# Optimization experiments

Measured on AMD Instinct MI355X. Metric: run time of the kernel, lower is better.

## Reference

```python
import jax, jax.numpy as jnp
import numpy as np

MODEL_DIM = 1024
BATCH, SEQ = 4, 2048


def setup_inputs() -> dict:
    key = jax.random.key(0)
    kx, kq, kk, kv = jax.random.split(key, 4)
    s = 1.0 / np.sqrt(MODEL_DIM)
    return {
        "x": jax.random.normal(kx, (BATCH, SEQ, MODEL_DIM), dtype=jnp.float32),
        "Wq": jax.random.normal(kq, (MODEL_DIM, MODEL_DIM), dtype=jnp.float32) * s,
        "Wk": jax.random.normal(kk, (MODEL_DIM, MODEL_DIM), dtype=jnp.float32) * s,
        "Wv": jax.random.normal(kv, (MODEL_DIM, MODEL_DIM), dtype=jnp.float32) * s,
    }


def reference(x, Wq, Wk, Wv):
    # nn.Linear(d, d, bias=False): y = x @ W.T ; W stored [out, in]
    q = jnp.einsum("bsd,ed->bse", x, Wq)
    k = jnp.einsum("bsd,ed->bse", x, Wk)
    v = jnp.einsum("bsd,ed->bse", x, Wv)
    scores = jnp.einsum("bqd,bkd->bqk", q, k) / jnp.sqrt(jnp.float32(MODEL_DIM))
    attn = jax.nn.softmax(scores, axis=-1)
    return jnp.einsum("bqk,bkd->bqd", attn, v)
```

## Files before the change

kernel.cpp:

```cpp
#include <hip/hip_runtime.h>
#include <hip/hip_bf16.h>


typedef short bf16x8_t __attribute__((ext_vector_type(8)));
typedef float f32x4_t __attribute__((ext_vector_type(4)));
typedef unsigned short u16x8_t __attribute__((ext_vector_type(8)));

static __device__ __forceinline__ unsigned short f2bf(float f) {
  __hip_bfloat16 h = __float2bfloat16(f);
  return *reinterpret_cast<unsigned short*>(&h);
}

#define GLOAD_LDS16(gp, lp)                                            \
  __builtin_amdgcn_global_load_lds(                                    \
      (const __attribute__((address_space(1))) void*)(gp),             \
      (__attribute__((address_space(3))) void*)(lp), 16, 0, 0)

__global__ __launch_bounds__(256) void cast_f32_bf16(
    const float* __restrict__ in, unsigned short* __restrict__ out, int n8) {
  int i = blockIdx.x * 256 + threadIdx.x;
  if (i >= n8) return;
  float4 a = ((const float4*)in)[i * 2];
  float4 b = ((const float4*)in)[i * 2 + 1];
  u16x8_t o;
  o[0] = f2bf(a.x); o[1] = f2bf(a.y); o[2] = f2bf(a.z); o[3] = f2bf(a.w);
  o[4] = f2bf(b.x); o[5] = f2bf(b.y); o[6] = f2bf(b.z); o[7] = f2bf(b.w);
  ((u16x8_t*)out)[i] = o;
}

__global__ __launch_bounds__(256) void cast_w3(
    const float* __restrict__ Wq, const float* __restrict__ Wk,
    const float* __restrict__ Wv, unsigned short* __restrict__ Wqk,
    unsigned short* __restrict__ Wvb) {
  int i = blockIdx.x * 256 + threadIdx.x;
  int seg = i >> 17;
  int local = i & 131071;
  const float* src = (seg == 0) ? Wq : ((seg == 1) ? Wk : Wv);
  unsigned short* dst =
      (seg == 0) ? Wqk : ((seg == 1) ? (Wqk + 1048576) : Wvb);
  float4 a = ((const float4*)src)[local * 2];
  float4 b = ((const float4*)src)[local * 2 + 1];
  u16x8_t o;
  o[0] = f2bf(a.x); o[1] = f2bf(a.y); o[2] = f2bf(a.z); o[3] = f2bf(a.w);
  o[4] = f2bf(b.x); o[5] = f2bf(b.y); o[6] = f2bf(b.z); o[7] = f2bf(b.w);
  ((u16x8_t*)dst)[local] = o;
}

__global__ __launch_bounds__(256) void zero_f32(float* __restrict__ p, int n) {
  int i = blockIdx.x * 256 + threadIdx.x;
  if (i < n) p[i] = 0.0f;
}

template <int EPI, int BN>
__global__ __launch_bounds__(512, 2) void gemm256p(
    const unsigned short* __restrict__ A, const unsigned short* __restrict__ B,
    void* __restrict__ Cv, float* __restrict__ rowsum, int K, int lda,
    int ldb, int ldc, long long sA, long long sB, long long sC, float alpha,
    int rsz) {
  constexpr int NBG = BN / 64;
  constexpr int NH = NBG / 2;
  constexpr int BL = BN / 128;
  constexpr int BNW = BN / 4;
  constexpr int ASZ = 256 * 64;
  constexpr int BSZ = BN * 64;

  __shared__ unsigned short lds[2][ASZ + BSZ];

  const int gx = gridDim.x, gy = gridDim.y;
  const int nwg = gx * gy * gridDim.z;
  const int orig = (blockIdx.z * gy + blockIdx.y) * gx + blockIdx.x;
  const int swz = (orig & 7) * (nwg >> 3) + (orig >> 3);
  const int bx = swz % gx;
  const int tmp = swz / gx;
  const int by = tmp % gy;
  const int z = tmp / gy;

  const int tid = threadIdx.x;
  const int lane = tid & 63;
  const int w = tid >> 6;
  const int wm = w >> 2, wn = w & 3;
  const int m0 = by * 256, n0 = bx * BN;

  A += (long long)z * sA;
  B += (long long)z * sB;

  int sta_row[2][2], sta_col[2][2], sta_lds[2][2];
#pragma unroll
  for (int mh = 0; mh < 2; ++mh)
#pragma unroll
    for (int i = 0; i < 2; ++i) {
      int j = w * 2 + i;
      int l0 = (j >> 3) * 1024 + mh * 512 + (j & 7) * 64;
      int lf = l0 + lane;
      int R = lf >> 3;
      sta_row[mh][i] = R;
      sta_col[mh][i] = ((lf & 7) ^ (R & 7)) * 8;
      sta_lds[mh][i] = l0 * 8;
    }
  int stb_row[2][BL], stb_col[2][BL], stb_lds[2][BL];
#pragma unroll
  for (int nh = 0; nh < 2; ++nh)
#pragma unroll
    for (int i = 0; i < BL; ++i) {
      int l0;
      if (BL == 2) {
        int j = w * 2 + i;
        l0 = (j >> 2) * 512 + nh * 256 + (j & 3) * 64;
      } else {
        int j = w;
        l0 = (j >> 1) * 256 + nh * 128 + (j & 1) * 64;
      }
      int lf = l0 + lane;
      int R = lf >> 3;
      stb_row[nh][i] = R;
      stb_col[nh][i] = ((lf & 7) ^ (R & 7)) * 8;
      stb_lds[nh][i] = ASZ + l0 * 8;
    }

  const int q = lane >> 4, rl = lane & 15;
  int aoff[8][2], boff[NBG][2];
#pragma unroll
  for (int tt = 0; tt < 8; ++tt)
#pragma unroll
    for (int ks = 0; ks < 2; ++ks) {
      int ra = wm * 128 + tt * 16 + rl;
      aoff[tt][ks] = ra * 64 + (((ks * 4 + q) ^ (ra & 7)) * 8);
    }
#pragma unroll
  for (int u = 0; u < NBG; ++u)
#pragma unroll
    for (int ks = 0; ks < 2; ++ks) {
      int rb = wn * BNW + u * 16 + rl;
      boff[u][ks] = ASZ + rb * 64 + (((ks * 4 + q) ^ (rb & 7)) * 8);
    }

  f32x4_t acc[8][NBG];
#pragma unroll
  for (int i = 0; i < 8; ++i)
#pragma unroll
    for (int j = 0; j < NBG; ++j) acc[i][j] = (f32x4_t){0.f, 0.f, 0.f, 0.f};

#define SA(BUFI, MH, K0)                                                    \
  {                                                                         \
    _Pragma("unroll") for (int i_ = 0; i_ < 2; ++i_)                        \
        GLOAD_LDS16(&A[(long long)(m0 + sta_row[MH][i_]) * lda + (K0) +     \
                       sta_col[MH][i_]],                                    \
                    &lds[BUFI][sta_lds[MH][i_]]);                           \
  }
#define SB(BUFI, NH_, K0)                                                   \
  {                                                                         \
    _Pragma("unroll") for (int i_ = 0; i_ < BL; ++i_)                       \
        GLOAD_LDS16(&B[(long long)(n0 + stb_row[NH_][i_]) * ldb + (K0) +    \
                       stb_col[NH_][i_]],                                   \
                    &lds[BUFI][stb_lds[NH_][i_]]);                          \
  }
#define LDAF(MH)                                                            \
  _Pragma("unroll") for (int i_ = 0; i_ < 4; ++i_)                          \
  _Pragma("unroll") for (int ks_ = 0; ks_ < 2; ++ks_)                       \
      af[i_][ks_] = *(const bf16x8_t*)&L[aoff[(MH)*4 + i_][ks_]];
#define LDBG(NH_)                                                           \
  _Pragma("unroll") for (int j_ = 0; j_ < NH; ++j_)                         \
  _Pragma("unroll") for (int ks_ = 0; ks_ < 2; ++ks_)                       \
      bg[j_][ks_] = *(const bf16x8_t*)&L[boff[(NH_)*NH + j_][ks_]];
#define PH_MFMA(MH, NH_)                                                    \
  __builtin_amdgcn_s_barrier();                                             \
  asm volatile("s_waitcnt lgkmcnt(0)" ::: "memory");                        \
  __builtin_amdgcn_sched_barrier(0);                                        \
  __builtin_amdgcn_s_setprio(1);                                            \
  _Pragma("unroll") for (int ks_ = 0; ks_ < 2; ++ks_)                       \
  _Pragma("unroll") for (int i_ = 0; i_ < 4; ++i_)                          \
  _Pragma("unroll") for (int j_ = 0; j_ < NH; ++j_)                         \
      acc[(MH)*4 + i_][(NH_)*NH + j_] =                                     \
          __builtin_amdgcn_mfma_f32_16x16x32_bf16(                          \
              af[i_][ks_], bg[j_][ks_], acc[(MH)*4 + i_][(NH_)*NH + j_],    \
              0, 0, 0);                                                     \
  __builtin_amdgcn_s_setprio(0);                                            \
  __builtin_amdgcn_sched_barrier(0);                                        \
  __builtin_amdgcn_s_barrier();                                             \
  __builtin_amdgcn_sched_barrier(0);

  const int NT = K >> 6;

  SA(0, 0, 0); SA(0, 1, 0); SB(0, 0, 0); SB(0, 1, 0);
  SA(1, 0, 64); SB(1, 1, 64);
  if (BL == 2)
    asm volatile("s_waitcnt vmcnt(4)" ::: "memory");
  else
    asm volatile("s_waitcnt vmcnt(3)" ::: "memory");
  __builtin_amdgcn_s_barrier();
  __builtin_amdgcn_sched_barrier(0);

  bf16x8_t af[4][2], bg[NH][2];

  for (int t = 0; t < NT; ++t) {
    const int bu = t & 1, nx = bu ^ 1;
    const unsigned short* L = lds[bu];
    const bool p1 = (t + 1 < NT), p2 = (t + 2 < NT);
    LDAF(0);
    LDBG(0);
    if (p1) SA(nx, 1, (t + 1) * 64);
    PH_MFMA(0, 0);
    LDBG(1);
    if (p1) SB(nx, 0, (t + 1) * 64);
    PH_MFMA(0, 1);
    LDAF(1);
    if (p2) SA(bu, 0, (t + 2) * 64);
    PH_MFMA(1, 1);
    LDBG(0);
    if (p2) {
      SB(bu, 1, (t + 2) * 64);
      if (BL == 2)
        asm volatile("s_waitcnt vmcnt(4)" ::: "memory");
      else
        asm volatile("s_waitcnt vmcnt(3)" ::: "memory");
    } else {
      asm volatile("s_waitcnt vmcnt(0)" ::: "memory");
    }
    PH_MFMA(1, 0);
  }

  if (EPI == 0) {
    unsigned short* C = (unsigned short*)Cv + (long long)z * sC;
#pragma unroll
    for (int tt = 0; tt < 8; ++tt)
#pragma unroll
      for (int u = 0; u < NBG; ++u)
#pragma unroll
        for (int j = 0; j < 4; ++j) {
          int row = m0 + wm * 128 + tt * 16 + q * 4 + j;
          int col = n0 + wn * BNW + u * 16 + rl;
          C[(long long)row * ldc + col] = f2bf(acc[tt][u][j] * alpha);
        }
  } else if (EPI == 1) {
    unsigned short* C = (unsigned short*)Cv + (long long)z * sC;
#pragma unroll
    for (int tt = 0; tt < 8; ++tt)
#pragma unroll
      for (int j = 0; j < 4; ++j) {
        int row = m0 + wm * 128 + tt * 16 + q * 4 + j;
        float sum = 0.f;
#pragma unroll
        for (int u = 0; u < NBG; ++u) {
          float e = __expf(acc[tt][u][j] * alpha);
          int col = n0 + wn * BNW + u * 16 + rl;
          C[(long long)row * ldc + col] = f2bf(e);
          sum += e;
        }
#pragma unroll
        for (int mk = 1; mk <= 8; mk <<= 1) sum += __shfl_xor(sum, mk);
        if (rl == 0) atomicAdd(&rowsum[z * rsz + row], sum);
      }
  } else {
    float* C = (float*)Cv + (long long)z * sC;
#pragma unroll
    for (int tt = 0; tt < 8; ++tt)
#pragma unroll
      for (int j = 0; j < 4; ++j) {
        int row = m0 + wm * 128 + tt * 16 + q * 4 + j;
        float inv = 1.0f / rowsum[z * rsz + row];
#pragma unroll
        for (int u = 0; u < NBG; ++u) {
          int col = n0 + wn * BNW + u * 16 + rl;
          C[(long long)row * ldc + col] = acc[tt][u][j] * inv;
        }
      }
  }
#undef SA
#undef SB
#undef LDAF
#undef LDBG
#undef PH_MFMA
}

__global__ __launch_bounds__(256) void gemm_nt128(
    const unsigned short* __restrict__ A, const unsigned short* __restrict__ B,
    unsigned short* __restrict__ C, int K, int lda, int ldb, int ldc) {
  __shared__ unsigned short As[128 * 64];
  __shared__ unsigned short Bs[128 * 64];

  const int gx = gridDim.x, gy = gridDim.y;
  const int nwg = gx * gy;
  const int orig = blockIdx.y * gx + blockIdx.x;
  const int swz = (orig & 7) * (nwg >> 3) + (orig >> 3);
  const int bx = swz % gx;
  const int by = swz / gx;

  const int tid = threadIdx.x;
  const int lane = tid & 63;
  const int w = tid >> 6;
  const int wm = w >> 1, wn = w & 1;
  const int m0 = by * 128;
  const int n0 = bx * 128;

  int srow[4], scol[4];
#pragma unroll
  for (int i = 0; i < 4; ++i) {
    int p = w * 256 + i * 64 + lane;
    int r = p >> 3;
    srow[i] = r;
    scol[i] = ((p & 7) ^ (r & 7)) * 8;
  }

  const int q = lane >> 4, rl = lane & 15;
  int aoff[4][2], boff[4][2];
#pragma unroll
  for (int t = 0; t < 4; ++t)
#pragma unroll
    for (int ks = 0; ks < 2; ++ks) {
      int ra = wm * 64 + t * 16 + rl;
      int ca = ks * 4 + q;
      aoff[t][ks] = ra * 64 + ((ca ^ (ra & 7)) * 8);
      int rb = wn * 64 + t * 16 + rl;
      boff[t][ks] = rb * 64 + ((ca ^ (rb & 7)) * 8);
    }

  f32x4_t acc[4][4];
#pragma unroll
  for (int i = 0; i < 4; ++i)
#pragma unroll
    for (int j = 0; j < 4; ++j) acc[i][j] = (f32x4_t){0.f, 0.f, 0.f, 0.f};

  for (int k0 = 0; k0 < K; k0 += 64) {
    __syncthreads();
#pragma unroll
    for (int i = 0; i < 4; ++i) {
      GLOAD_LDS16(&A[(long long)(m0 + srow[i]) * lda + k0 + scol[i]],
                  &As[(w * 4 + i) * 512]);
      GLOAD_LDS16(&B[(long long)(n0 + srow[i]) * ldb + k0 + scol[i]],
                  &Bs[(w * 4 + i) * 512]);
    }
    __syncthreads();

#pragma unroll
    for (int ks = 0; ks < 2; ++ks) {
      bf16x8_t af[4], bgv[4];
#pragma unroll
      for (int t = 0; t < 4; ++t) af[t] = *(const bf16x8_t*)&As[aoff[t][ks]];
#pragma unroll
      for (int u = 0; u < 4; ++u) bgv[u] = *(const bf16x8_t*)&Bs[boff[u][ks]];
#pragma unroll
      for (int i = 0; i < 4; ++i)
#pragma unroll
        for (int j = 0; j < 4; ++j)
          acc[i][j] = __builtin_amdgcn_mfma_f32_16x16x32_bf16(
              af[i], bgv[j], acc[i][j], 0, 0, 0);
    }
  }

#pragma unroll
  for (int t = 0; t < 4; ++t)
#pragma unroll
    for (int u = 0; u < 4; ++u)
#pragma unroll
      for (int j = 0; j < 4; ++j) {
        int row = m0 + wm * 64 + t * 16 + q * 4 + j;
        int col = n0 + wn * 64 + u * 16 + rl;
        C[(long long)row * ldc + col] = f2bf(acc[t][u][j]);
      }
}

extern "C" void kernel_launch(void* const* d_in, const int* in_sizes, int n_in,
                              void* d_out, int out_size, void* d_ws,
                              size_t ws_size, hipStream_t stream) {
  const float* x = (const float*)d_in[0];
  const float* Wq = (const float*)d_in[1];
  const float* Wk = (const float*)d_in[2];
  const float* Wv = (const float*)d_in[3];
  float* out = (float*)d_out;

  unsigned short* xb = (unsigned short*)d_ws;
  unsigned short* Wqk = xb + 8388608;
  unsigned short* Wvb = Wqk + 2097152;
  unsigned short* Cqk = Wvb + 1048576;
  unsigned short* VTb = Cqk + 16777216;
  unsigned short* Scb = VTb + 8388608;
  float* rowsumf = (float*)(Scb + 16777216);

  const dim3 blk(256);
  const dim3 blk512(512);

  cast_f32_bf16<<<4096, blk, 0, stream>>>(x, xb, 1048576);
  cast_w3<<<1536, blk, 0, stream>>>(Wq, Wk, Wv, Wqk, Wvb);
  zero_f32<<<32, blk, 0, stream>>>(rowsumf, 8192);

  gemm256p<0, 256><<<dim3(8, 32, 1), blk512, 0, stream>>>(
      xb, Wqk, Cqk, nullptr, 1024, 1024, 1024, 2048, 0, 0, 0, 1.0f, 0);

  gemm_nt128<<<dim3(64, 8), blk, 0, stream>>>(Wvb, xb, VTb, 1024, 1024, 1024,
                                              8192);

  gemm256p<1, 256><<<dim3(8, 8, 4), blk512, 0, stream>>>(
      Cqk, Cqk + 1024, Scb, rowsumf, 1024, 2048, 2048, 2048,
      (long long)2048 * 2048, (long long)2048 * 2048, (long long)2048 * 2048,
      0.03125f, 2048);

  gemm256p<2, 128><<<dim3(8, 8, 4), blk512, 0, stream>>>(
      Scb, VTb, out, rowsumf, 2048, 2048, 8192, 1024,
      (long long)2048 * 2048, 2048, (long long)2048 * 1024, 1.0f, 2048);
}
```

Measured before the change: 164.0 us.

## Software-pipeline LDS fragment reads across phases and fold rowsum zeroing into weight cast

The GEMM main loop is restructured so LDS fragment reads for the next phase, and for the next K-tile, are issued before the current phase's MFMAs. It uses extra register buffers (afA/afB, bgX0/bgX1/bgY), a loop unrolled by two, and one barrier per phase instead of two. The aim is to hide LDS read latency behind MFMA work and cut barrier overhead. Prefetch addresses wrap modulo NT, so the last tiles issue redundant loads, and the loop assumes NT is even. The separate zero_f32 launch is also removed by zeroing rowsum in extra blocks of cast_w3, saving one kernel launch. The extra register buffers raise register pressure.

```diff
diff --git a/kernel.cpp b/kernel.cpp
--- a/kernel.cpp
+++ b/kernel.cpp
@@ -31,9 +31,18 @@
 __global__ __launch_bounds__(256) void cast_w3(
     const float* __restrict__ Wq, const float* __restrict__ Wk,
     const float* __restrict__ Wv, unsigned short* __restrict__ Wqk,
-    unsigned short* __restrict__ Wvb) {
+    unsigned short* __restrict__ Wvb, float* __restrict__ rowsum) {
   int i = blockIdx.x * 256 + threadIdx.x;
   int seg = i >> 17;
+  if (seg >= 3) {
+    int l = i - 393216;
+    if (l < 1024) {
+      float4 z = {0.f, 0.f, 0.f, 0.f};
+      ((float4*)rowsum)[l * 2] = z;
+      ((float4*)rowsum)[l * 2 + 1] = z;
+    }
+    return;
+  }
   int local = i & 131071;
   const float* src = (seg == 0) ? Wq : ((seg == 1) ? Wk : Wv);
   unsigned short* dst =
@@ -44,11 +53,6 @@
   o[0] = f2bf(a.x); o[1] = f2bf(a.y); o[2] = f2bf(a.z); o[3] = f2bf(a.w);
   o[4] = f2bf(b.x); o[5] = f2bf(b.y); o[6] = f2bf(b.z); o[7] = f2bf(b.w);
   ((u16x8_t*)dst)[local] = o;
-}
-
-__global__ __launch_bounds__(256) void zero_f32(float* __restrict__ p, int n) {
-  int i = blockIdx.x * 256 + threadIdx.x;
-  if (i < n) p[i] = 0.0f;
 }
 
 template <int EPI, int BN>
@@ -140,6 +144,8 @@
 #pragma unroll
     for (int j = 0; j < NBG; ++j) acc[i][j] = (f32x4_t){0.f, 0.f, 0.f, 0.f};
 
+  bf16x8_t afA[4][2], afB[4][2], bgY[NH][2], bgX0[NH][2], bgX1[NH][2];
+
 #define SA(BUFI, MH, K0)                                                    \
   {                                                                         \
     _Pragma("unroll") for (int i_ = 0; i_ < 2; ++i_)                        \
@@ -154,17 +160,15 @@
                        stb_col[NH_][i_]],                                   \
                     &lds[BUFI][stb_lds[NH_][i_]]);                          \
   }
-#define LDAF(MH)                                                            \
+#define RD_AF(DST, L, MH)                                                   \
   _Pragma("unroll") for (int i_ = 0; i_ < 4; ++i_)                          \
   _Pragma("unroll") for (int ks_ = 0; ks_ < 2; ++ks_)                       \
-      af[i_][ks_] = *(const bf16x8_t*)&L[aoff[(MH)*4 + i_][ks_]];
-#define LDBG(NH_)                                                           \
+      DST[i_][ks_] = *(const bf16x8_t*)&(L)[aoff[(MH)*4 + i_][ks_]];
+#define RD_BG(DST, L, NH_)                                                  \
   _Pragma("unroll") for (int j_ = 0; j_ < NH; ++j_)                         \
   _Pragma("unroll") for (int ks_ = 0; ks_ < 2; ++ks_)                       \
-      bg[j_][ks_] = *(const bf16x8_t*)&L[boff[(NH_)*NH + j_][ks_]];
-#define PH_MFMA(MH, NH_)                                                    \
-  __builtin_amdgcn_s_barrier();                                             \
-  asm volatile("s_waitcnt lgkmcnt(0)" ::: "memory");                        \
+      DST[j_][ks_] = *(const bf16x8_t*)&(L)[boff[(NH_)*NH + j_][ks_]];
+#define MM(MH, NH_, AF, BG)                                                 \
   __builtin_amdgcn_sched_barrier(0);                                        \
   __builtin_amdgcn_s_setprio(1);                                            \
   _Pragma("unroll") for (int ks_ = 0; ks_ < 2; ++ks_)                       \
@@ -172,52 +176,65 @@
   _Pragma("unroll") for (int j_ = 0; j_ < NH; ++j_)                         \
       acc[(MH)*4 + i_][(NH_)*NH + j_] =                                     \
           __builtin_amdgcn_mfma_f32_16x16x32_bf16(                          \
-              af[i_][ks_], bg[j_][ks_], acc[(MH)*4 + i_][(NH_)*NH + j_],    \
+              AF[i_][ks_], BG[j_][ks_], acc[(MH)*4 + i_][(NH_)*NH + j_],    \
               0, 0, 0);                                                     \
-  __builtin_amdgcn_s_setprio(0);                                            \
-  __builtin_amdgcn_sched_barrier(0);                                        \
-  __builtin_amdgcn_s_barrier();                                             \
+  __builtin_amdgcn_s_setprio(0);
+
+#define VMC_PH1()                                                           \
+  if constexpr (BL == 2) {                                                  \
+    asm volatile("s_waitcnt vmcnt(4)" ::: "memory");                        \
+  } else {                                                                  \
+    asm volatile("s_waitcnt vmcnt(3)" ::: "memory");                        \
+  }                                                                         \
   __builtin_amdgcn_sched_barrier(0);
+#define VMC_PH2()                                                           \
+  asm volatile("s_waitcnt vmcnt(2)" ::: "memory");                          \
+  __builtin_amdgcn_sched_barrier(0);
+
+#define TILE(T, BU, NX, BGXc, BGXn)                                         \
+  {                                                                         \
+    const unsigned short* Lb = lds[BU];                                     \
+    const unsigned short* Ln = lds[NX];                                     \
+    const int k1 = (((T) + 1 < NT) ? ((T) + 1) : ((T) + 1 - NT)) * 64;      \
+    const int k2 = (((T) + 2 < NT) ? ((T) + 2) : ((T) + 2 - NT)) * 64;      \
+                                                                   \
+    __builtin_amdgcn_s_barrier();                                           \
+    RD_BG(bgY, Lb, 1);                                                      \
+    SA(NX, 1, k1);                                                          \
+    MM(0, 0, afA, BGXc);                                                    \
+                                                                   \
+    __builtin_amdgcn_s_barrier();                                           \
+    RD_AF(afB, Lb, 1);                                                      \
+    SB(NX, 0, k1);                                                          \
+    MM(0, 1, afA, bgY);                                                     \
+    VMC_PH1();                                                              \
+                                                                   \
+    __builtin_amdgcn_s_barrier();                                           \
+    RD_AF(afA, Ln, 0);                                                      \
+    SA(BU, 0, k2);                                                          \
+    MM(1, 1, afB, bgY);                                                     \
+    VMC_PH2();                                                              \
+                                                                   \
+    __builtin_amdgcn_s_barrier();                                           \
+    RD_BG(BGXn, Ln, 0);                                                     \
+    SB(BU, 1, k2);                                                          \
+    MM(1, 0, afB, BGXc);                                                    \
+  }
 
   const int NT = K >> 6;
 
   SA(0, 0, 0); SA(0, 1, 0); SB(0, 0, 0); SB(0, 1, 0);
   SA(1, 0, 64); SB(1, 1, 64);
-  if (BL == 2)
-    asm volatile("s_waitcnt vmcnt(4)" ::: "memory");
-  else
-    asm volatile("s_waitcnt vmcnt(3)" ::: "memory");
+  VMC_PH1();
   __builtin_amdgcn_s_barrier();
-  __builtin_amdgcn_sched_barrier(0);
-
-  bf16x8_t af[4][2], bg[NH][2];
-
-  for (int t = 0; t < NT; ++t) {
-    const int bu = t & 1, nx = bu ^ 1;
-    const unsigned short* L = lds[bu];
-    const bool p1 = (t + 1 < NT), p2 = (t + 2 < NT);
-    LDAF(0);
-    LDBG(0);
-    if (p1) SA(nx, 1, (t + 1) * 64);
-    PH_MFMA(0, 0);
-    LDBG(1);
-    if (p1) SB(nx, 0, (t + 1) * 64);
-    PH_MFMA(0, 1);
-    LDAF(1);
-    if (p2) SA(bu, 0, (t + 2) * 64);
-    PH_MFMA(1, 1);
-    LDBG(0);
-    if (p2) {
-      SB(bu, 1, (t + 2) * 64);
-      if (BL == 2)
-        asm volatile("s_waitcnt vmcnt(4)" ::: "memory");
-      else
-        asm volatile("s_waitcnt vmcnt(3)" ::: "memory");
-    } else {
-      asm volatile("s_waitcnt vmcnt(0)" ::: "memory");
-    }
-    PH_MFMA(1, 0);
-  }
+  RD_AF(afA, lds[0], 0);
+  RD_BG(bgX0, lds[0], 0);
+
+  for (int t = 0; t < NT; t += 2) {
+    TILE(t, 0, 1, bgX0, bgX1);
+    TILE(t + 1, 1, 0, bgX1, bgX0);
+  }
+  asm volatile("s_waitcnt vmcnt(0)" ::: "memory");
 
   if (EPI == 0) {
     unsigned short* C = (unsigned short*)Cv + (long long)z * sC;
@@ -267,9 +284,12 @@
   }
 #undef SA
 #undef SB
-#undef LDAF
-#undef LDBG
-#undef PH_MFMA
+#undef RD_AF
+#undef RD_BG
+#undef MM
+#undef VMC_PH1
+#undef VMC_PH2
+#undef TILE
 }
 
 __global__ __launch_bounds__(256) void gemm_nt128(
@@ -380,8 +400,7 @@
   const dim3 blk512(512);
 
   cast_f32_bf16<<<4096, blk, 0, stream>>>(x, xb, 1048576);
-  cast_w3<<<1536, blk, 0, stream>>>(Wq, Wk, Wv, Wqk, Wvb);
-  zero_f32<<<32, blk, 0, stream>>>(rowsumf, 8192);
+  cast_w3<<<1540, blk, 0, stream>>>(Wq, Wk, Wv, Wqk, Wvb, rowsumf);
 
   gemm256p<0, 256><<<dim3(8, 32, 1), blk512, 0, stream>>>(
       xb, Wqk, Cqk, nullptr, 1024, 1024, 1024, 2048, 0, 0, 0, 1.0f, 0);
```

After: 308.2 us. 87.9% more time.

## Fuse cast/zero kernels and restructure GEMM prefetch with deeper vmcnt waits

Applied to the files above, without the earlier changes.

Merges the x cast, weight cast and rowsum zeroing into one launch to cut launch overhead. In the main GEMM the K loop is unrolled by two with a TILE macro, the order of A/B half-tile prefetches is changed, and the global-load waits move to a looser vmcnt placed mid-tile, so more loads stay in flight across MFMA phases. The risk is that a wrong vmcnt count lets the kernel read LDS data that has not arrived yet. The unrolled loop also assumes the tile count NT is even.

```diff
diff --git a/kernel.cpp b/kernel.cpp
--- a/kernel.cpp
+++ b/kernel.cpp
@@ -16,39 +16,39 @@
       (const __attribute__((address_space(1))) void*)(gp),             \
       (__attribute__((address_space(3))) void*)(lp), 16, 0, 0)
 
-__global__ __launch_bounds__(256) void cast_f32_bf16(
-    const float* __restrict__ in, unsigned short* __restrict__ out, int n8) {
+__global__ __launch_bounds__(256) void cast_all(
+    const float* __restrict__ x, const float* __restrict__ Wq,
+    const float* __restrict__ Wk, const float* __restrict__ Wv,
+    unsigned short* __restrict__ xb, unsigned short* __restrict__ Wqk,
+    unsigned short* __restrict__ Wvb, float* __restrict__ rowsum) {
   int i = blockIdx.x * 256 + threadIdx.x;
-  if (i >= n8) return;
-  float4 a = ((const float4*)in)[i * 2];
-  float4 b = ((const float4*)in)[i * 2 + 1];
-  u16x8_t o;
-  o[0] = f2bf(a.x); o[1] = f2bf(a.y); o[2] = f2bf(a.z); o[3] = f2bf(a.w);
-  o[4] = f2bf(b.x); o[5] = f2bf(b.y); o[6] = f2bf(b.z); o[7] = f2bf(b.w);
-  ((u16x8_t*)out)[i] = o;
-}
-
-__global__ __launch_bounds__(256) void cast_w3(
-    const float* __restrict__ Wq, const float* __restrict__ Wk,
-    const float* __restrict__ Wv, unsigned short* __restrict__ Wqk,
-    unsigned short* __restrict__ Wvb) {
-  int i = blockIdx.x * 256 + threadIdx.x;
-  int seg = i >> 17;
-  int local = i & 131071;
-  const float* src = (seg == 0) ? Wq : ((seg == 1) ? Wk : Wv);
-  unsigned short* dst =
-      (seg == 0) ? Wqk : ((seg == 1) ? (Wqk + 1048576) : Wvb);
+  const float* src;
+  unsigned short* dst;
+  int local;
+  if (i < 1048576) {
+    src = x; dst = xb; local = i;
+  } else {
+    int j = i - 1048576;
+    int seg = j >> 17;
+    if (seg >= 3) {
+      int l = j - 393216;
+      if (l < 1024) {
+        float4 zz = {0.f, 0.f, 0.f, 0.f};
+        ((float4*)rowsum)[l * 2] = zz;
+        ((float4*)rowsum)[l * 2 + 1] = zz;
+      }
+      return;
+    }
+    local = j & 131071;
+    src = (seg == 0) ? Wq : ((seg == 1) ? Wk : Wv);
+    dst = (seg == 0) ? Wqk : ((seg == 1) ? (Wqk + 1048576) : Wvb);
+  }
   float4 a = ((const float4*)src)[local * 2];
   float4 b = ((const float4*)src)[local * 2 + 1];
   u16x8_t o;
   o[0] = f2bf(a.x); o[1] = f2bf(a.y); o[2] = f2bf(a.z); o[3] = f2bf(a.w);
   o[4] = f2bf(b.x); o[5] = f2bf(b.y); o[6] = f2bf(b.z); o[7] = f2bf(b.w);
   ((u16x8_t*)dst)[local] = o;
-}
-
-__global__ __launch_bounds__(256) void zero_f32(float* __restrict__ p, int n) {
-  int i = blockIdx.x * 256 + threadIdx.x;
-  if (i < n) p[i] = 0.0f;
 }
 
 template <int EPI, int BN>
@@ -179,44 +179,62 @@
   __builtin_amdgcn_s_barrier();                                             \
   __builtin_amdgcn_sched_barrier(0);
 
+#define VMC_A()                                                             \
+  if constexpr (BL == 2) {                                                  \
+    asm volatile("s_waitcnt vmcnt(8)" ::: "memory");                        \
+  } else {                                                                  \
+    asm volatile("s_waitcnt vmcnt(6)" ::: "memory");                        \
+  }                                                                         \
+  __builtin_amdgcn_sched_barrier(0);
+#define VMC_B()                                                             \
+  if constexpr (BL == 2) {                                                  \
+    asm volatile("s_waitcnt vmcnt(6)" ::: "memory");                        \
+  } else {                                                                  \
+    asm volatile("s_waitcnt vmcnt(5)" ::: "memory");                        \
+  }                                                                         \
+  __builtin_amdgcn_sched_barrier(0);
+#define VMC_0()                                                             \
+  asm volatile("s_waitcnt vmcnt(0)" ::: "memory");                          \
+  __builtin_amdgcn_sched_barrier(0);
+
+#define TILE(T, BU, NX)                                                     \
+  {                                                                         \
+    const unsigned short* L = lds[BU];                                      \
+    const int k1 = ((T) + 1) * 64;                                          \
+    const int k2 = ((T) + 2) * 64;                                          \
+    const bool p1 = ((T) + 1 < NT), p2 = ((T) + 2 < NT);                    \
+    bf16x8_t af[4][2], bg[NH][2];                                           \
+                                                           \
+    LDAF(0);                                                                \
+    LDBG(0);                                                                \
+    if (p1) SB(NX, 0, k1);                                                  \
+    PH_MFMA(0, 0);                                                          \
+                                                           \
+    LDBG(1);                                                                \
+    if (p1) SA(NX, 1, k1);                                                  \
+    if (p2) { VMC_A(); } else { VMC_0(); }                                  \
+    PH_MFMA(0, 1);                                                          \
+                                                           \
+    LDAF(1);                                                                \
+    if (p2) SA(BU, 0, k2);                                                  \
+    PH_MFMA(1, 1);                                                          \
+                                                           \
+    LDBG(0);                                                                \
+    if (p2) { SB(BU, 1, k2); VMC_B(); } else { VMC_0(); }                   \
+    PH_MFMA(1, 0);                                                          \
+  }
+
   const int NT = K >> 6;
 
-  SA(0, 0, 0); SA(0, 1, 0); SB(0, 0, 0); SB(0, 1, 0);
+  SA(0, 0, 0); SB(0, 0, 0); SB(0, 1, 0); SA(0, 1, 0);
   SA(1, 0, 64); SB(1, 1, 64);
-  if (BL == 2)
-    asm volatile("s_waitcnt vmcnt(4)" ::: "memory");
-  else
-    asm volatile("s_waitcnt vmcnt(3)" ::: "memory");
+  VMC_B();
   __builtin_amdgcn_s_barrier();
   __builtin_amdgcn_sched_barrier(0);
 
-  bf16x8_t af[4][2], bg[NH][2];
-
-  for (int t = 0; t < NT; ++t) {
-    const int bu = t & 1, nx = bu ^ 1;
-    const unsigned short* L = lds[bu];
-    const bool p1 = (t + 1 < NT), p2 = (t + 2 < NT);
-    LDAF(0);
-    LDBG(0);
-    if (p1) SA(nx, 1, (t + 1) * 64);
-    PH_MFMA(0, 0);
-    LDBG(1);
-    if (p1) SB(nx, 0, (t + 1) * 64);
-    PH_MFMA(0, 1);
-    LDAF(1);
-    if (p2) SA(bu, 0, (t + 2) * 64);
-    PH_MFMA(1, 1);
-    LDBG(0);
-    if (p2) {
-      SB(bu, 1, (t + 2) * 64);
-      if (BL == 2)
-        asm volatile("s_waitcnt vmcnt(4)" ::: "memory");
-      else
-        asm volatile("s_waitcnt vmcnt(3)" ::: "memory");
-    } else {
-      asm volatile("s_waitcnt vmcnt(0)" ::: "memory");
-    }
-    PH_MFMA(1, 0);
+  for (int t = 0; t < NT; t += 2) {
+    TILE(t, 0, 1);
+    TILE(t + 1, 1, 0);
   }
 
   if (EPI == 0) {
@@ -270,6 +288,10 @@
 #undef LDAF
 #undef LDBG
 #undef PH_MFMA
+#undef VMC_A
+#undef VMC_B
+#undef VMC_0
+#undef TILE
 }
 
 __global__ __launch_bounds__(256) void gemm_nt128(
@@ -379,9 +401,7 @@
   const dim3 blk(256);
   const dim3 blk512(512);
 
-  cast_f32_bf16<<<4096, blk, 0, stream>>>(x, xb, 1048576);
-  cast_w3<<<1536, blk, 0, stream>>>(Wq, Wk, Wv, Wqk, Wvb);
-  zero_f32<<<32, blk, 0, stream>>>(rowsumf, 8192);
+  cast_all<<<5636, blk, 0, stream>>>(x, Wq, Wk, Wv, xb, Wqk, Wvb, rowsumf);
 
   gemm256p<0, 256><<<dim3(8, 32, 1), blk512, 0, stream>>>(
       xb, Wqk, Cqk, nullptr, 1024, 1024, 1024, 2048, 0, 0, 0, 1.0f, 0);
@@ -391,8 +411,8 @@
 
   gemm256p<1, 256><<<dim3(8, 8, 4), blk512, 0, stream>>>(
       Cqk, Cqk + 1024, Scb, rowsumf, 1024, 2048, 2048, 2048,
-      (long long)2048 * 2048, (long long)2048 * 2048, (long long)2048 * 2048,
-      0.03125f, 2048);
+      (long long)2048 * 2048, (long long)2048 * 2048,
+      (long long)2048 * 2048, 0.03125f, 2048);
 
   gemm256p<2, 128><<<dim3(8, 8, 4), blk512, 0, stream>>>(
       Scb, VTb, out, rowsumf, 2048, 2048, 8192, 1024,
```

New measurement: 160.8 us. 1.02x faster.
